# Kernel tuning notes

Hardware: AMD Instinct MI355X
Metric: run time of the kernel (lower is better)

Reference implementation:

```python
import jax, jax.numpy as jnp
import numpy as np
import math

CHUNK = 33554432  # 2**25, power of two so the 2^n index space is fully covered


def setup_inputs() -> dict:
    key = jax.random.key(0)
    k1, k2 = jax.random.split(key)
    phi_vals = jax.random.normal(k1, (CHUNK,), dtype=jnp.float32)
    weights = jax.random.uniform(k2, (CHUNK,), dtype=jnp.float32)
    return {"phi_vals": phi_vals, "weights": weights}


def reference(phi_vals, weights):
    # Analytic closed form of the PennyLane circuit:
    #   n index qubits in uniform superposition, Hadamard-sandwiched ancilla h,
    #   per-index controlled-RZ(2*w_p*phi_p) on a |0> target kicks phase
    #   e^{-i w_p phi_p} onto the h=1 branch of index state p.
    #   <Z_h> = (sum_p cos(w_p * phi_p) + (2^n - C)) / 2^n
    C = phi_vals.shape[0]
    n = int(math.ceil(math.log2(C)))
    N = 2 ** n
    s = jnp.sum(jnp.cos(weights * phi_vals))
    return (s + jnp.float32(N - C)) / jnp.float32(N)
```

## Files before the change

### kernel.cpp

```cpp
#include <hip/hip_runtime.h>


#define RBLOCKS 2048
#define RTHREADS 256

__global__ __launch_bounds__(RTHREADS) void qs_partial_kernel(
    const float* __restrict__ phi, const float* __restrict__ w,
    float* __restrict__ partials, int n4, int n) {
    const float4* __restrict__ p4 = (const float4*)phi;
    const float4* __restrict__ w4 = (const float4*)w;

    float acc = 0.0f;
    const int idx    = blockIdx.x * blockDim.x + threadIdx.x;
    const int stride = gridDim.x * blockDim.x;

    int i = idx;
    for (; i + 3 * stride < n4; i += 4 * stride) {
        float4 a0 = p4[i];
        float4 a1 = p4[i + stride];
        float4 a2 = p4[i + 2 * stride];
        float4 a3 = p4[i + 3 * stride];
        float4 b0 = w4[i];
        float4 b1 = w4[i + stride];
        float4 b2 = w4[i + 2 * stride];
        float4 b3 = w4[i + 3 * stride];
        acc += __cosf(a0.x * b0.x) + __cosf(a0.y * b0.y)
             + __cosf(a0.z * b0.z) + __cosf(a0.w * b0.w);
        acc += __cosf(a1.x * b1.x) + __cosf(a1.y * b1.y)
             + __cosf(a1.z * b1.z) + __cosf(a1.w * b1.w);
        acc += __cosf(a2.x * b2.x) + __cosf(a2.y * b2.y)
             + __cosf(a2.z * b2.z) + __cosf(a2.w * b2.w);
        acc += __cosf(a3.x * b3.x) + __cosf(a3.y * b3.y)
             + __cosf(a3.z * b3.z) + __cosf(a3.w * b3.w);
    }
    for (; i < n4; i += stride) {
        float4 a = p4[i];
        float4 b = w4[i];
        acc += __cosf(a.x * b.x) + __cosf(a.y * b.y)
             + __cosf(a.z * b.z) + __cosf(a.w * b.w);
    }
    if (idx == 0) {
        for (int j = n4 * 4; j < n; ++j) acc += __cosf(phi[j] * w[j]);
    }

    #pragma unroll
    for (int off = 32; off > 0; off >>= 1)
        acc += __shfl_down(acc, off, 64);

    __shared__ float smem[RTHREADS / 64];
    int lane = threadIdx.x & 63;
    int wid  = threadIdx.x >> 6;
    if (lane == 0) smem[wid] = acc;
    __syncthreads();
    if (threadIdx.x == 0) {
        float t = 0.0f;
        #pragma unroll
        for (int k = 0; k < RTHREADS / 64; ++k) t += smem[k];
        partials[blockIdx.x] = t;
    }
}

__global__ __launch_bounds__(1024) void qs_final_kernel(
    const float* __restrict__ partials, float* __restrict__ out,
    int nb, float addend, float inv_n) {
    float acc = 0.0f;
    for (int i = threadIdx.x; i < nb; i += blockDim.x) acc += partials[i];

    #pragma unroll
    for (int off = 32; off > 0; off >>= 1)
        acc += __shfl_down(acc, off, 64);

    __shared__ float smem[1024 / 64];
    int lane = threadIdx.x & 63;
    int wid  = threadIdx.x >> 6;
    if (lane == 0) smem[wid] = acc;
    __syncthreads();
    if (threadIdx.x == 0) {
        float t = 0.0f;
        #pragma unroll
        for (int k = 0; k < 1024 / 64; ++k) t += smem[k];
        out[0] = (t + addend) * inv_n;
    }
}

extern "C" void kernel_launch(void* const* d_in, const int* in_sizes, int n_in,
                              void* d_out, int out_size, void* d_ws, size_t ws_size,
                              hipStream_t stream) {
    const float* phi = (const float*)d_in[0];
    const float* w   = (const float*)d_in[1];
    float* out       = (float*)d_out;
    float* partials  = (float*)d_ws;

    int n  = in_sizes[0];
    int n4 = n >> 2;

    long long N = 1;
    while (N < (long long)n) N <<= 1;
    float addend = (float)(N - (long long)n);
    float inv_n  = 1.0f / (float)N;

    qs_partial_kernel<<<RBLOCKS, RTHREADS, 0, stream>>>(phi, w, partials, n4, n);
    qs_final_kernel<<<1, 1024, 0, stream>>>(partials, out, RBLOCKS, addend, inv_n);
}
```

Before: 281.6 us.

## Use blocked per-block spans with nontemporal vector loads in reduction

Each block now covers one contiguous span of the input instead of a grid-strided set of chunks. Loads use nontemporal builtins on ext_vector types, and the loop unroll drops from four to two. The aim is better DRAM locality and less cache pollution on a streaming read of 256 MB. The trade-off is fewer loads in flight per thread, which could lower achieved bandwidth.

```diff
diff --git a/kernel.cpp b/kernel.cpp
--- a/kernel.cpp
+++ b/kernel.cpp
@@ -4,42 +4,38 @@
 #define RBLOCKS 2048
 #define RTHREADS 256
 
+typedef float v4f __attribute__((ext_vector_type(4)));
+
 __global__ __launch_bounds__(RTHREADS) void qs_partial_kernel(
     const float* __restrict__ phi, const float* __restrict__ w,
     float* __restrict__ partials, int n4, int n) {
-    const float4* __restrict__ p4 = (const float4*)phi;
-    const float4* __restrict__ w4 = (const float4*)w;
+    const v4f* __restrict__ p4 = (const v4f*)phi;
+    const v4f* __restrict__ w4 = (const v4f*)w;
+
+    const int span  = (n4 + (int)gridDim.x - 1) / (int)gridDim.x;
+    const int start = (int)blockIdx.x * span;
+    const int lim   = (start + span < n4) ? (start + span) : n4;
 
     float acc = 0.0f;
-    const int idx    = blockIdx.x * blockDim.x + threadIdx.x;
-    const int stride = gridDim.x * blockDim.x;
+    int i = start + (int)threadIdx.x;
 
-    int i = idx;
-    for (; i + 3 * stride < n4; i += 4 * stride) {
-        float4 a0 = p4[i];
-        float4 a1 = p4[i + stride];
-        float4 a2 = p4[i + 2 * stride];
-        float4 a3 = p4[i + 3 * stride];
-        float4 b0 = w4[i];
-        float4 b1 = w4[i + stride];
-        float4 b2 = w4[i + 2 * stride];
-        float4 b3 = w4[i + 3 * stride];
+    for (; i + RTHREADS < lim; i += 2 * RTHREADS) {
+        v4f a0 = __builtin_nontemporal_load(p4 + i);
+        v4f a1 = __builtin_nontemporal_load(p4 + i + RTHREADS);
+        v4f b0 = __builtin_nontemporal_load(w4 + i);
+        v4f b1 = __builtin_nontemporal_load(w4 + i + RTHREADS);
         acc += __cosf(a0.x * b0.x) + __cosf(a0.y * b0.y)
              + __cosf(a0.z * b0.z) + __cosf(a0.w * b0.w);
         acc += __cosf(a1.x * b1.x) + __cosf(a1.y * b1.y)
              + __cosf(a1.z * b1.z) + __cosf(a1.w * b1.w);
-        acc += __cosf(a2.x * b2.x) + __cosf(a2.y * b2.y)
-             + __cosf(a2.z * b2.z) + __cosf(a2.w * b2.w);
-        acc += __cosf(a3.x * b3.x) + __cosf(a3.y * b3.y)
-             + __cosf(a3.z * b3.z) + __cosf(a3.w * b3.w);
     }
-    for (; i < n4; i += stride) {
-        float4 a = p4[i];
-        float4 b = w4[i];
+    for (; i < lim; i += RTHREADS) {
+        v4f a = __builtin_nontemporal_load(p4 + i);
+        v4f b = __builtin_nontemporal_load(w4 + i);
         acc += __cosf(a.x * b.x) + __cosf(a.y * b.y)
              + __cosf(a.z * b.z) + __cosf(a.w * b.w);
     }
-    if (idx == 0) {
+    if (blockIdx.x == 0 && threadIdx.x == 0) {
         for (int j = n4 * 4; j < n; ++j) acc += __cosf(phi[j] * w[j]);
     }
 
```

New measurement: 248.5 us. 1.13x faster.
